# Kernel tuning notes

Hardware: AMD Instinct MI355X
Metric: run time of the kernel (lower is better)

The kernel has to match this reference:

```python
import jax, jax.numpy as jnp
import numpy as np

DIM = 384
NUM_HEADS = 12
WIN = 7
N = WIN * WIN  # 49
B = 4096


def _relative_position_index():
    coords = np.stack(np.meshgrid(np.arange(WIN), np.arange(WIN), indexing='ij'))  # (2,W,W)
    cf = coords.reshape(2, -1)  # (2, N)
    rel = cf[:, :, None] - cf[:, None, :]  # (2, N, N)
    rel = rel.transpose(1, 2, 0).astype(np.int64)  # (N, N, 2)
    rel[:, :, 0] += WIN - 1
    rel[:, :, 1] += WIN - 1
    rel[:, :, 0] *= 2 * WIN - 1
    return jnp.asarray(rel.sum(-1), dtype=jnp.int32)  # (N, N)


def setup_inputs() -> dict:
    key = jax.random.key(0)
    ks = jax.random.split(key, 6)
    x = jax.random.normal(ks[0], (B, N, DIM), dtype=jnp.float32)
    mask = jnp.zeros((B, N, N), dtype=jnp.float32)
    qkv_w = jax.random.normal(ks[1], (3 * DIM, DIM), dtype=jnp.float32) * 0.02
    qkv_b = jnp.zeros((3 * DIM,), dtype=jnp.float32)
    proj_w = jax.random.normal(ks[2], (DIM, DIM), dtype=jnp.float32) * 0.02
    proj_b = jnp.zeros((DIM,), dtype=jnp.float32)
    bias_table = jax.random.normal(ks[3], ((2 * WIN - 1) ** 2, NUM_HEADS), dtype=jnp.float32) * 0.02
    rel_index = _relative_position_index()
    return {"x": x, "mask": mask, "qkv_w": qkv_w, "qkv_b": qkv_b,
            "proj_w": proj_w, "proj_b": proj_b, "bias_table": bias_table,
            "rel_index": rel_index}


def reference(x, mask, qkv_w, qkv_b, proj_w, proj_b, bias_table, rel_index):
    B_, n, C = x.shape
    H = NUM_HEADS
    d = C // H
    scale = d ** (-0.5)
    # fused qkv projection: (B_, n, 3, H, d)
    qkv = (x @ qkv_w.T + qkv_b).reshape(B_, n, 3, H, d)
    qkv = jnp.transpose(qkv, (2, 0, 3, 1, 4))  # (3, B_, H, n, d)
    q, k, v = qkv[0], qkv[1], qkv[2]
    attn = jnp.einsum('bhnd,bhmd->bhnm', q * scale, k)  # (B_, H, n, n)
    # relative position bias gather: (n, n, H) -> (H, n, n)
    rel_bias = jnp.transpose(bias_table[rel_index], (2, 0, 1))
    attn = attn + rel_bias[None] + mask[:, None]
    attn = jax.nn.softmax(attn, axis=-1)
    out = jnp.einsum('bhnm,bhmd->bnhd', attn, v).reshape(B_, n, C)
    return out @ proj_w.T + proj_b
```

## Files before the change

kernel.cpp:

```cpp
#include <hip/hip_runtime.h>
#include <hip/hip_bf16.h>

#define NWIN   4096
#define NTOK   49
#define CDIM   384
#define NHEAD  12
#define QKVN   1152

typedef __attribute__((ext_vector_type(8))) short bf16x8;
typedef __attribute__((ext_vector_type(4))) short bf16x4;
typedef __attribute__((ext_vector_type(4))) float f32x4;
typedef __attribute__((ext_vector_type(2))) unsigned int u32x2;
typedef unsigned int u32;
typedef unsigned short u16;

static __device__ __forceinline__ u16 f2bf(float f) {
  union { float f; u32 u; } w; w.f = f;
  u32 r = w.u + 0x7fffu + ((w.u >> 16) & 1u);
  return (u16)(r >> 16);
}
static __device__ __forceinline__ float blo(u32 v) {
  union { u32 u; float f; } w; w.u = v << 16; return w.f;
}
static __device__ __forceinline__ float bhi(u32 v) {
  union { u32 u; float f; } w; w.u = v & 0xffff0000u; return w.f;
}
static __device__ __forceinline__ u32 cvtpk2(float lo, float hi) {
  u32 r; asm("v_cvt_pk_bf16_f32 %0, %1, %2" : "=v"(r) : "v"(lo), "v"(hi));
  return r;
}
static __device__ __forceinline__ void gld_lds16(const u16* g, u16* l) {
  __builtin_amdgcn_global_load_lds((const __attribute__((address_space(1))) u32*)g,
                                   (__attribute__((address_space(3))) u32*)l, 16, 0, 0);
}

__global__ void k_prep(const float* __restrict__ qkv_w, const float* __restrict__ proj_w,
                       const float* __restrict__ btab, const int* __restrict__ ridx,
                       u16* __restrict__ wq, u16* __restrict__ wp, u32* __restrict__ rbp)
{
  const int n1 = QKVN * CDIM;
  const int n2 = CDIM * CDIM;
  const int n3 = NHEAD * NTOK * 26;
  for (int i = blockIdx.x * blockDim.x + threadIdx.x; i < n1 + n2 + n3;
       i += gridDim.x * blockDim.x) {
    if (i < n1) {
      wq[i] = f2bf(qkv_w[i]);
    } else if (i < n1 + n2) {
      wp[i - n1] = f2bf(proj_w[i - n1]);
    } else {
      int t = i - n1 - n2;
      int h = t / (NTOK * 26); int rem = t % (NTOK * 26);
      int r = rem / 26, p = rem % 26;
      float lo = 0.f, hi = 0.f;
      if (p < 25) {
        lo = btab[ridx[r * NTOK + 2 * p] * NHEAD + h];
        if (2 * p + 1 < NTOK) hi = btab[ridx[r * NTOK + 2 * p + 1] * NHEAD + h];
      }
      rbp[(h * NTOK + r) * 26 + p] = (u32)f2bf(lo) | ((u32)f2bf(hi) << 16);
    }
  }
}

__global__ void k_convx(const float* __restrict__ x, u16* __restrict__ xb, long n8)
{
  long i = (long)blockIdx.x * blockDim.x + threadIdx.x;
  long stride = (long)gridDim.x * blockDim.x;
  for (; i < n8; i += stride) {
    const float4* p = (const float4*)x + i * 2;
    float4 a = p[0], b = p[1];
    u32 w0 = (u32)f2bf(a.x) | ((u32)f2bf(a.y) << 16);
    u32 w1 = (u32)f2bf(a.z) | ((u32)f2bf(a.w) << 16);
    u32 w2 = (u32)f2bf(b.x) | ((u32)f2bf(b.y) << 16);
    u32 w3 = (u32)f2bf(b.z) | ((u32)f2bf(b.w) << 16);
    uint4 v; v.x = w0; v.y = w1; v.z = w2; v.w = w3;
    ((uint4*)xb)[i] = v;
  }
}

template<bool OUT_BF16>
__global__ __launch_bounds__(256, 4)
void k_gemm(const u16* __restrict__ A, int lda,
            const u16* __restrict__ Bt, const float* __restrict__ bias,
            void* __restrict__ C, int ldc, int K, int tiles_n)
{
  __shared__ alignas(16) u16 As[128 * 64];
  __shared__ alignas(16) u16 Bs[128 * 64];
  const int tid = threadIdx.x;
  const int w = tid >> 6, l = tid & 63;

  const int nwg = (int)gridDim.x;
  const int xcd = (int)blockIdx.x & 7, idx8 = (int)blockIdx.x >> 3;
  const int q8 = nwg >> 3, r8w = nwg & 7;
  const int lid = (xcd < r8w ? xcd * (q8 + 1) : r8w * (q8 + 1) + (xcd - r8w) * q8) + idx8;

  const int tm = lid / tiles_n, tn = lid % tiles_n;
  const int wm = (w >> 1) * 64, wn = (w & 1) * 64;
  const long arow0 = (long)tm * 128;
  const long brow0 = (long)tn * 128;
  const int r8 = l >> 3;
  const int c8 = ((l & 7) ^ r8) * 8;

  f32x4 acc[4][4];
  const f32x4 z = {0.f, 0.f, 0.f, 0.f};
#pragma unroll
  for (int m = 0; m < 4; ++m)
#pragma unroll
    for (int n = 0; n < 4; ++n) acc[m][n] = z;

  for (int kk = 0; kk < K; kk += 64) {
    __syncthreads();
#pragma unroll
    for (int q = 0; q < 4; ++q) {
      int ra = w * 32 + q * 8;
      gld_lds16(A  + (arow0 + ra + r8) * (long)lda + kk + c8, &As[ra * 64]);
      gld_lds16(Bt + (brow0 + ra + r8) * (long)K   + kk + c8, &Bs[ra * 64]);
    }
    __syncthreads();
#pragma unroll
    for (int ks = 0; ks < 2; ++ks) {
      const int ko = ks * 32 + (l >> 4) * 8;
      const int rl = l & 15;
      const int sa = (rl & 7) * 8;
      bf16x8 af[4], bfr[4];
#pragma unroll
      for (int m = 0; m < 4; ++m) af[m]  = *(const bf16x8*)&As[(wm + m * 16 + rl) * 64 + (ko ^ sa)];
#pragma unroll
      for (int n = 0; n < 4; ++n) bfr[n] = *(const bf16x8*)&Bs[(wn + n * 16 + rl) * 64 + (ko ^ sa)];
#pragma unroll
      for (int m = 0; m < 4; ++m)
#pragma unroll
        for (int n = 0; n < 4; ++n)
          acc[m][n] = __builtin_amdgcn_mfma_f32_16x16x32_bf16(bfr[n], af[m], acc[m][n], 0, 0, 0);
    }
  }

  const int li = l & 15, g4 = (l >> 4) * 4;
  float4 bv[4];
#pragma unroll
  for (int n = 0; n < 4; ++n)
    bv[n] = *(const float4*)&bias[tn * 128 + wn + n * 16 + g4];
#pragma unroll
  for (int m = 0; m < 4; ++m) {
    const long row = arow0 + wm + m * 16 + li;
#pragma unroll
    for (int n = 0; n < 4; ++n) {
      const long colb = brow0 + wn + n * 16 + g4;
      float v0 = acc[m][n][0] + bv[n].x;
      float v1 = acc[m][n][1] + bv[n].y;
      float v2 = acc[m][n][2] + bv[n].z;
      float v3 = acc[m][n][3] + bv[n].w;
      if (OUT_BF16) {
        u32x2 pk;
        pk[0] = (u32)f2bf(v0) | ((u32)f2bf(v1) << 16);
        pk[1] = (u32)f2bf(v2) | ((u32)f2bf(v3) << 16);
        *(u32x2*)((u16*)C + row * ldc + colb) = pk;
      } else {
        float4 pk; pk.x = v0; pk.y = v1; pk.z = v2; pk.w = v3;
        *(float4*)((float*)C + row * ldc + colb) = pk;
      }
    }
  }
}

__global__ __launch_bounds__(384, 2)
void k_attn(u16* __restrict__ qkv, const float* __restrict__ maskc,
            const u32* __restrict__ rbp)
{
  __shared__ alignas(16) u16 Vt[6][32 * 64];
  __shared__ alignas(16) u32 mp[NTOK * 26];
  const int tid = threadIdx.x;
  const int w = tid >> 6, l = tid & 63;
  const int g = l >> 4, li = l & 15;
  const int id = blockIdx.x;
  const int logical = (id & 7) * ((int)gridDim.x >> 3) + (id >> 3);
  const int bl = logical >> 1, hg = logical & 1;
  const int h = hg * 6 + w;
  const long rowbase = (long)bl * NTOK;
  const float scale = 0.17677669529663687f;

  u16* vt = Vt[w];
  {
    const int jj = l >> 2;
    const int d0 = (l & 3) * 8;
#pragma unroll
    for (int it = 0; it < 4; ++it) {
      int j = it * 16 + jj;
      bf16x8 vv = {0, 0, 0, 0, 0, 0, 0, 0};
      if (j < NTOK)
        vv = *(const bf16x8*)(qkv + (rowbase + j) * QKVN + 2 * CDIM + h * 32 + d0);
#pragma unroll
      for (int t = 0; t < 8; ++t)
        vt[(d0 + t) * 64 + (j ^ (t << 3))] = (u16)vv[t];
    }
  }
  for (int e = tid; e < NTOK * 25; e += 384) {
    int i = e / 25, p = e - i * 25;
    const float* mrow = maskc + (long)bl * (NTOK * NTOK) + i * NTOK;
    float lo = mrow[2 * p];
    float hi = (2 * p + 1 < NTOK) ? mrow[2 * p + 1] : 0.f;
    mp[i * 26 + p] = (u32)f2bf(lo) | ((u32)f2bf(hi) << 16);
  }
  if (tid < NTOK) mp[tid * 26 + 25] = 0;
  __syncthreads();

  bf16x8 kf[4], qf[4];
#pragma unroll
  for (int jm = 0; jm < 4; ++jm) {
    int rj = jm * 16 + li; if (rj >= NTOK) rj = NTOK - 1;
    kf[jm] = *(const bf16x8*)(qkv + (rowbase + rj) * QKVN + CDIM + h * 32 + g * 8);
  }
#pragma unroll
  for (int in = 0; in < 4; ++in) {
    int ri = in * 16 + li; if (ri >= NTOK) ri = NTOK - 1;
    qf[in] = *(const bf16x8*)(qkv + (rowbase + ri) * QKVN + h * 32 + g * 8);
  }
  const f32x4 z = {0.f, 0.f, 0.f, 0.f};
  f32x4 st[4][4];
#pragma unroll
  for (int jm = 0; jm < 4; ++jm)
#pragma unroll
    for (int in = 0; in < 4; ++in)
      st[jm][in] = __builtin_amdgcn_mfma_f32_16x16x32_bf16(kf[jm], qf[in], z, 0, 0, 0);

#pragma unroll
  for (int jm = 0; jm < 4; ++jm) {
    int p0 = 8 * jm + 2 * g; if (p0 > 24) p0 = 24;
#pragma unroll
    for (int in = 0; in < 4; ++in) {
      int i = 16 * in + li; int ic = i < NTOK ? i : NTOK - 1;
      const u32* bp = rbp + (h * NTOK + ic) * 26 + p0;
      u32 b0w = bp[0], b1w = bp[1];
      u32 m0w = mp[ic * 26 + p0], m1w = mp[ic * 26 + p0 + 1];
      st[jm][in][0] = st[jm][in][0] * scale + blo(b0w) + blo(m0w);
      st[jm][in][1] = st[jm][in][1] * scale + bhi(b0w) + bhi(m0w);
      st[jm][in][2] = st[jm][in][2] * scale + blo(b1w) + blo(m1w);
      st[jm][in][3] = st[jm][in][3] * scale + bhi(b1w) + bhi(m1w);
    }
  }

  float inv[4];
#pragma unroll
  for (int in = 0; in < 4; ++in) {
    float mx = -3.0e38f;
#pragma unroll
    for (int jm = 0; jm < 4; ++jm)
#pragma unroll
      for (int rr = 0; rr < 4; ++rr) mx = fmaxf(mx, st[jm][in][rr]);
    mx = fmaxf(mx, __shfl_xor(mx, 16));
    mx = fmaxf(mx, __shfl_xor(mx, 32));
    float sum = 0.f;
#pragma unroll
    for (int jm = 0; jm < 4; ++jm) {
      const int j0 = 16 * jm + 4 * g;
#pragma unroll
      for (int rr = 0; rr < 4; ++rr) {
        float p = (j0 + rr < NTOK) ? __expf(st[jm][in][rr] - mx) : 0.f;
        st[jm][in][rr] = p; sum += p;
      }
    }
    sum += __shfl_xor(sum, 16);
    sum += __shfl_xor(sum, 32);
    inv[in] = (16 * in + li < NTOK) ? (1.f / sum) : 0.f;
  }

  f32x4 oacc[4][2];
#pragma unroll
  for (int im = 0; im < 4; ++im)
#pragma unroll
    for (int dn = 0; dn < 2; ++dn) oacc[im][dn] = z;
  const int sw = (li & 7) << 3;
#pragma unroll
  for (int ks = 0; ks < 2; ++ks) {
    union { bf16x4 h[2]; bf16x8 v8; } vf[2];
#pragma unroll
    for (int dn = 0; dn < 2; ++dn) {
      const u16* vrow = &vt[(16 * dn + li) * 64];
      vf[dn].h[0] = *(const bf16x4*)&vrow[(32 * ks + 4 * g) ^ sw];
      vf[dn].h[1] = *(const bf16x4*)&vrow[(32 * ks + 16 + 4 * g) ^ sw];
    }
#pragma unroll
    for (int im = 0; im < 4; ++im) {
      union { u32 w[4]; bf16x8 v8; } pa;
      pa.w[0] = cvtpk2(st[2 * ks][im][0] * inv[im], st[2 * ks][im][1] * inv[im]);
      pa.w[1] = cvtpk2(st[2 * ks][im][2] * inv[im], st[2 * ks][im][3] * inv[im]);
      pa.w[2] = cvtpk2(st[2 * ks + 1][im][0] * inv[im], st[2 * ks + 1][im][1] * inv[im]);
      pa.w[3] = cvtpk2(st[2 * ks + 1][im][2] * inv[im], st[2 * ks + 1][im][3] * inv[im]);
#pragma unroll
      for (int dn = 0; dn < 2; ++dn)
        oacc[im][dn] = __builtin_amdgcn_mfma_f32_16x16x32_bf16(pa.v8, vf[dn].v8, oacc[im][dn], 0, 0, 0);
    }
  }

#pragma unroll
  for (int im = 0; im < 4; ++im) {
#pragma unroll
    for (int rr = 0; rr < 4; ++rr) {
      const int i = 16 * im + 4 * g + rr;
      if (i < NTOK) {
        u16* orow = qkv + (rowbase + i) * QKVN + h * 32;
#pragma unroll
        for (int dn = 0; dn < 2; ++dn)
          orow[16 * dn + li] = f2bf(oacc[im][dn][rr]);
      }
    }
  }
}

extern "C" void kernel_launch(void* const* d_in, const int* in_sizes, int n_in,
                              void* d_out, int out_size, void* d_ws, size_t ws_size,
                              hipStream_t stream)
{
  const float* x      = (const float*)d_in[0];
  const float* mask   = (const float*)d_in[1];
  const float* qkv_w  = (const float*)d_in[2];
  const float* qkv_b  = (const float*)d_in[3];
  const float* proj_w = (const float*)d_in[4];
  const float* proj_b = (const float*)d_in[5];
  const float* btab   = (const float*)d_in[6];
  const int*   ridx   = (const int*)d_in[7];
  float* out = (float*)d_out;

  auto need = [](int bc) -> size_t {
    return (size_t)bc * NTOK * QKVN * 2
         + (size_t)bc * NTOK * CDIM * 2
         + (size_t)QKVN * CDIM * 2
         + (size_t)CDIM * CDIM * 2
         + (size_t)NHEAD * NTOK * 26 * 4
         + 1024;
  };
  int BC = NWIN;
  while (BC > 128 && need(BC) > ws_size) BC >>= 1;

  char* p = (char*)d_ws;
  u16* qkvbuf = (u16*)p;  p += (size_t)BC * NTOK * QKVN * 2;
  u16* xb     = (u16*)p;  p += (size_t)BC * NTOK * CDIM * 2;
  u16* wq     = (u16*)p;  p += (size_t)QKVN * CDIM * 2;
  u16* wp     = (u16*)p;  p += (size_t)CDIM * CDIM * 2;
  u32* rbp    = (u32*)p;

  k_prep<<<512, 256, 0, stream>>>(qkv_w, proj_w, btab, ridx, wq, wp, rbp);

  const int nc = NWIN / BC;
  const int Mc = BC * NTOK;
  for (int c = 0; c < nc; ++c) {
    const float* xc = x + (size_t)c * Mc * CDIM;
    k_convx<<<2048, 256, 0, stream>>>(xc, xb, (long)Mc * CDIM / 8);
    k_gemm<true><<<(Mc / 128) * 9, 256, 0, stream>>>(
        xb, CDIM, wq, qkv_b, (void*)qkvbuf, QKVN, CDIM, 9);
    k_attn<<<BC * 2, 384, 0, stream>>>(
        qkvbuf, mask + (size_t)c * BC * NTOK * NTOK, rbp);
    k_gemm<false><<<(Mc / 128) * 3, 256, 0, stream>>>(
        qkvbuf, QKVN, wp, proj_b, (void*)(out + (size_t)c * Mc * CDIM), CDIM, CDIM, 3);
  }
}
```

Measured before the change: 737.7 us.

## Restructure attention kernel to process query blocks sequentially with early Q/K loads

Moves the Q and K fragment loads ahead of the V transpose and mask staging so global latency overlaps that shared-memory work. Restructures the score/softmax/PV loop to handle one 16-row query block at a time, cutting the live score registers from 16 f32x4 tiles to 4 and preloading all V fragments up front. Wraps the MFMA sections in s_setprio to favour matrix issue across waves. The gain depends on whether the lower register pressure and the reordering improve overlap at the existing 2-blocks-per-CU occupancy.

```diff
diff --git a/kernel.cpp b/kernel.cpp
--- a/kernel.cpp
+++ b/kernel.cpp
@@ -178,6 +178,18 @@
   const long rowbase = (long)bl * NTOK;
   const float scale = 0.17677669529663687f;
 
+  bf16x8 kf[4], qf[4];
+#pragma unroll
+  for (int jm = 0; jm < 4; ++jm) {
+    int rj = jm * 16 + li; if (rj >= NTOK) rj = NTOK - 1;
+    kf[jm] = *(const bf16x8*)(qkv + (rowbase + rj) * QKVN + CDIM + h * 32 + g * 8);
+  }
+#pragma unroll
+  for (int in = 0; in < 4; ++in) {
+    int ri = in * 16 + li; if (ri >= NTOK) ri = NTOK - 1;
+    qf[in] = *(const bf16x8*)(qkv + (rowbase + ri) * QKVN + h * 32 + g * 8);
+  }
+
   u16* vt = Vt[w];
   {
     const int jj = l >> 2;
@@ -203,49 +215,52 @@
   if (tid < NTOK) mp[tid * 26 + 25] = 0;
   __syncthreads();
 
-  bf16x8 kf[4], qf[4];
-#pragma unroll
-  for (int jm = 0; jm < 4; ++jm) {
-    int rj = jm * 16 + li; if (rj >= NTOK) rj = NTOK - 1;
-    kf[jm] = *(const bf16x8*)(qkv + (rowbase + rj) * QKVN + CDIM + h * 32 + g * 8);
-  }
+  const int sw = (li & 7) << 3;
+  union { bf16x4 hh[2]; bf16x8 v8; } vf[2][2];
+#pragma unroll
+  for (int ks = 0; ks < 2; ++ks)
+#pragma unroll
+    for (int dn = 0; dn < 2; ++dn) {
+      const u16* vrow = &vt[(16 * dn + li) * 64];
+      vf[ks][dn].hh[0] = *(const bf16x4*)&vrow[(32 * ks + 4 * g) ^ sw];
+      vf[ks][dn].hh[1] = *(const bf16x4*)&vrow[(32 * ks + 16 + 4 * g) ^ sw];
+    }
+
+  const f32x4 z = {0.f, 0.f, 0.f, 0.f};
+  f32x4 oacc[4][2];
+#pragma unroll
+  for (int im = 0; im < 4; ++im)
+#pragma unroll
+    for (int dn = 0; dn < 2; ++dn) oacc[im][dn] = z;
+
 #pragma unroll
   for (int in = 0; in < 4; ++in) {
-    int ri = in * 16 + li; if (ri >= NTOK) ri = NTOK - 1;
-    qf[in] = *(const bf16x8*)(qkv + (rowbase + ri) * QKVN + h * 32 + g * 8);
-  }
-  const f32x4 z = {0.f, 0.f, 0.f, 0.f};
-  f32x4 st[4][4];
-#pragma unroll
-  for (int jm = 0; jm < 4; ++jm)
-#pragma unroll
-    for (int in = 0; in < 4; ++in)
-      st[jm][in] = __builtin_amdgcn_mfma_f32_16x16x32_bf16(kf[jm], qf[in], z, 0, 0, 0);
-
-#pragma unroll
-  for (int jm = 0; jm < 4; ++jm) {
-    int p0 = 8 * jm + 2 * g; if (p0 > 24) p0 = 24;
-#pragma unroll
-    for (int in = 0; in < 4; ++in) {
-      int i = 16 * in + li; int ic = i < NTOK ? i : NTOK - 1;
+    __builtin_amdgcn_s_setprio(1);
+    f32x4 s[4];
+#pragma unroll
+    for (int jm = 0; jm < 4; ++jm)
+      s[jm] = __builtin_amdgcn_mfma_f32_16x16x32_bf16(kf[jm], qf[in], z, 0, 0, 0);
+    __builtin_amdgcn_s_setprio(0);
+
+    const int i = 16 * in + li;
+    const int ic = i < NTOK ? i : NTOK - 1;
+#pragma unroll
+    for (int jm = 0; jm < 4; ++jm) {
+      int p0 = 8 * jm + 2 * g; if (p0 > 24) p0 = 24;
       const u32* bp = rbp + (h * NTOK + ic) * 26 + p0;
       u32 b0w = bp[0], b1w = bp[1];
       u32 m0w = mp[ic * 26 + p0], m1w = mp[ic * 26 + p0 + 1];
-      st[jm][in][0] = st[jm][in][0] * scale + blo(b0w) + blo(m0w);
-      st[jm][in][1] = st[jm][in][1] * scale + bhi(b0w) + bhi(m0w);
-      st[jm][in][2] = st[jm][in][2] * scale + blo(b1w) + blo(m1w);
-      st[jm][in][3] = st[jm][in][3] * scale + bhi(b1w) + bhi(m1w);
-    }
-  }
-
-  float inv[4];
-#pragma unroll
-  for (int in = 0; in < 4; ++in) {
+      s[jm][0] = s[jm][0] * scale + blo(b0w) + blo(m0w);
+      s[jm][1] = s[jm][1] * scale + bhi(b0w) + bhi(m0w);
+      s[jm][2] = s[jm][2] * scale + blo(b1w) + blo(m1w);
+      s[jm][3] = s[jm][3] * scale + bhi(b1w) + bhi(m1w);
+    }
+
     float mx = -3.0e38f;
 #pragma unroll
     for (int jm = 0; jm < 4; ++jm)
 #pragma unroll
-      for (int rr = 0; rr < 4; ++rr) mx = fmaxf(mx, st[jm][in][rr]);
+      for (int rr = 0; rr < 4; ++rr) mx = fmaxf(mx, s[jm][rr]);
     mx = fmaxf(mx, __shfl_xor(mx, 16));
     mx = fmaxf(mx, __shfl_xor(mx, 32));
     float sum = 0.f;
@@ -254,41 +269,27 @@
       const int j0 = 16 * jm + 4 * g;
 #pragma unroll
       for (int rr = 0; rr < 4; ++rr) {
-        float p = (j0 + rr < NTOK) ? __expf(st[jm][in][rr] - mx) : 0.f;
-        st[jm][in][rr] = p; sum += p;
+        float p = (j0 + rr < NTOK) ? __expf(s[jm][rr] - mx) : 0.f;
+        s[jm][rr] = p; sum += p;
       }
     }
     sum += __shfl_xor(sum, 16);
     sum += __shfl_xor(sum, 32);
-    inv[in] = (16 * in + li < NTOK) ? (1.f / sum) : 0.f;
-  }
-
-  f32x4 oacc[4][2];
-#pragma unroll
-  for (int im = 0; im < 4; ++im)
-#pragma unroll
-    for (int dn = 0; dn < 2; ++dn) oacc[im][dn] = z;
-  const int sw = (li & 7) << 3;
-#pragma unroll
-  for (int ks = 0; ks < 2; ++ks) {
-    union { bf16x4 h[2]; bf16x8 v8; } vf[2];
-#pragma unroll
-    for (int dn = 0; dn < 2; ++dn) {
-      const u16* vrow = &vt[(16 * dn + li) * 64];
-      vf[dn].h[0] = *(const bf16x4*)&vrow[(32 * ks + 4 * g) ^ sw];
-      vf[dn].h[1] = *(const bf16x4*)&vrow[(32 * ks + 16 + 4 * g) ^ sw];
-    }
-#pragma unroll
-    for (int im = 0; im < 4; ++im) {
-      union { u32 w[4]; bf16x8 v8; } pa;
-      pa.w[0] = cvtpk2(st[2 * ks][im][0] * inv[im], st[2 * ks][im][1] * inv[im]);
-      pa.w[1] = cvtpk2(st[2 * ks][im][2] * inv[im], st[2 * ks][im][3] * inv[im]);
-      pa.w[2] = cvtpk2(st[2 * ks + 1][im][0] * inv[im], st[2 * ks + 1][im][1] * inv[im]);
-      pa.w[3] = cvtpk2(st[2 * ks + 1][im][2] * inv[im], st[2 * ks + 1][im][3] * inv[im]);
+    const float inv = (i < NTOK) ? (1.f / sum) : 0.f;
+
+    __builtin_amdgcn_s_setprio(1);
+#pragma unroll
+    for (int ks = 0; ks < 2; ++ks) {
+      union { u32 ww[4]; bf16x8 v8; } pa;
+      pa.ww[0] = cvtpk2(s[2 * ks][0] * inv, s[2 * ks][1] * inv);
+      pa.ww[1] = cvtpk2(s[2 * ks][2] * inv, s[2 * ks][3] * inv);
+      pa.ww[2] = cvtpk2(s[2 * ks + 1][0] * inv, s[2 * ks + 1][1] * inv);
+      pa.ww[3] = cvtpk2(s[2 * ks + 1][2] * inv, s[2 * ks + 1][3] * inv);
 #pragma unroll
       for (int dn = 0; dn < 2; ++dn)
-        oacc[im][dn] = __builtin_amdgcn_mfma_f32_16x16x32_bf16(pa.v8, vf[dn].v8, oacc[im][dn], 0, 0, 0);
-    }
+        oacc[in][dn] = __builtin_amdgcn_mfma_f32_16x16x32_bf16(pa.v8, vf[ks][dn].v8, oacc[in][dn], 0, 0, 0);
+    }
+    __builtin_amdgcn_s_setprio(0);
   }
 
 #pragma unroll
```

Result: no change. 749.0 us (+1.5%).
